# Kernel optimization log

Hardware: AMD Instinct MI355X
Metric: run time of the kernel (lower is better)

Reference implementation:

```python
import jax, jax.numpy as jnp
import numpy as np

H, DM, N, K, R = 768, 1536, 16, 4, 48  # hidden, intermediate, state, conv kernel, dt rank
B, L = 2, 1024


def _silu(x):
    return x * jax.nn.sigmoid(x)


def _causal_conv(x, w, b):
    # x: [B, D, L]; w: [D, K] depthwise; causal left-pad K-1 (matches causal_conv1d_fn)
    out = jax.lax.conv_general_dilated(
        x, w[:, None, :], window_strides=(1,), padding=[(K - 1, 0)],
        feature_group_count=w.shape[0], dimension_numbers=('NCH', 'OIH', 'NCH'))
    return out + b[None, :, None]


def _selective_scan(u, delta, A, Bm, Cm, Dp, gate):
    # u/delta/gate: [B, D, L]; A: [D, N]; Bm/Cm: [B, L, N]; Dp: [D]
    dA = jnp.exp(delta[:, :, :, None] * A[None, :, None, :])              # [B,D,L,N]
    dBu = delta[:, :, :, None] * Bm[:, None, :, :] * u[:, :, :, None]      # [B,D,L,N]
    dA_t = jnp.moveaxis(dA, 2, 0)    # [L,B,D,N]
    dBu_t = jnp.moveaxis(dBu, 2, 0)  # [L,B,D,N]
    C_t = jnp.moveaxis(Cm, 1, 0)     # [L,B,N]

    def step(x, inp):
        a, bu, c = inp
        x = a * x + bu                               # [B,D,N]
        y = jnp.einsum('bdn,bn->bd', x, c)
        return x, y

    x0 = jnp.zeros(dA_t.shape[1:], dA_t.dtype)
    _, ys = jax.lax.scan(step, x0, (dA_t, dBu_t, C_t))
    y = jnp.moveaxis(ys, 0, 2) + u * Dp[None, :, None]   # [B,D,L]
    return y * _silu(gate)


def _branch(conv_out, gate, xw, dtw, dtb, Alog, Dp):
    # conv_out/gate: [B, D, L]
    ssm = jnp.einsum('bdl,pd->blp', conv_out, xw)        # [B,L,R+2N]
    ts, Bm, Cm = ssm[..., :R], ssm[..., R:R + N], ssm[..., R + N:]
    delta = jax.nn.softplus(jnp.einsum('dr,blr->bdl', dtw, ts) + dtb[None, :, None])
    A = -jnp.exp(Alog)
    return _selective_scan(conv_out, delta, A, Bm, Cm, Dp, gate)


def setup_inputs() -> dict:
    key = jax.random.key(0)
    ks = jax.random.split(key, 12)
    s = 0.02
    hidden_states = jax.random.normal(ks[0], (B, L, H), jnp.float32)
    in_proj_w = jax.random.normal(ks[1], (2 * DM, H), jnp.float32) * s
    conv_w = jax.random.normal(ks[2], (DM, K), jnp.float32) * 0.3
    conv_b = jax.random.normal(ks[3], (DM,), jnp.float32) * s
    x_proj_w = jax.random.normal(ks[4], (R + 2 * N, DM), jnp.float32) * s
    dt_proj_w = jax.random.normal(ks[5], (DM, R), jnp.float32) * s
    dt_proj_b = -4.0 + 0.1 * jax.random.normal(ks[6], (DM,), jnp.float32)
    x_proj_back_w = jax.random.normal(ks[7], (R + 2 * N, DM), jnp.float32) * s
    dt_proj_back_w = jax.random.normal(ks[8], (DM, R), jnp.float32) * s
    dt_proj_back_b = -4.0 + 0.1 * jax.random.normal(ks[9], (DM,), jnp.float32)
    A_log = jnp.log(jnp.broadcast_to(jnp.arange(1, N + 1, dtype=jnp.float32)[None, :], (DM, N)))
    A_log_back = A_log
    D = jnp.ones((DM,), jnp.float32)
    D_back = jnp.ones((DM,), jnp.float32)
    out_proj_w = jax.random.normal(ks[10], (H, DM), jnp.float32) * s
    return {
        'hidden_states': hidden_states, 'in_proj_w': in_proj_w,
        'conv_w': conv_w, 'conv_b': conv_b,
        'x_proj_w': x_proj_w, 'dt_proj_w': dt_proj_w, 'dt_proj_b': dt_proj_b,
        'x_proj_back_w': x_proj_back_w, 'dt_proj_back_w': dt_proj_back_w,
        'dt_proj_back_b': dt_proj_back_b, 'A_log': A_log, 'A_log_back': A_log_back,
        'D': D, 'D_back': D_back, 'out_proj_w': out_proj_w,
    }


def reference(hidden_states, in_proj_w, conv_w, conv_b, x_proj_w, dt_proj_w,
              dt_proj_b, x_proj_back_w, dt_proj_back_w, dt_proj_back_b,
              A_log, A_log_back, D, D_back, out_proj_w):
    proj = jnp.einsum('blh,ph->bpl', hidden_states, in_proj_w)  # [B,2D,L]
    x, gate = proj[:, :DM], proj[:, DM:]
    conv_out = _silu(_causal_conv(x, conv_w, conv_b))           # [B,D,L]
    # forward-direction scan
    y_f = _branch(conv_out, gate, x_proj_w, dt_proj_w, dt_proj_b, A_log, D)
    # backward-direction scan on time-flipped conv output and gate
    y_b = _branch(conv_out[:, :, ::-1], gate[:, :, ::-1], x_proj_back_w,
                  dt_proj_back_w, dt_proj_back_b, A_log_back, D_back)
    y = y_f + y_b[:, :, ::-1]
    return jnp.einsum('bdl,hd->blh', y, out_proj_w)
```

## Files before the change

### kernel.cpp

```cpp
#include <hip/hip_runtime.h>
#include <math.h>

constexpr int cH  = 768;
constexpr int cDM = 1536;
constexpr int cN  = 16;
constexpr int cR  = 48;
constexpr int cB  = 2;
constexpr int cL  = 1024;
constexpr int cPS = 160;
constexpr int cCK = 8;

typedef unsigned short u16;
typedef __attribute__((ext_vector_type(8))) short bf16x8;
typedef __attribute__((ext_vector_type(4))) float f32x4;

__device__ __forceinline__ u16 f2bf(float f) {
    unsigned u = __float_as_uint(f);
    u += 0x7FFF + ((u >> 16) & 1);
    return (u16)(u >> 16);
}
__device__ __forceinline__ float bf2f(u16 h) {
    return __uint_as_float((unsigned)h << 16);
}

__device__ __forceinline__ float row16_sum(float y) {
    int v;
    v = __builtin_amdgcn_update_dpp(0, __float_as_int(y), 0xB1, 0xF, 0xF, true);
    y += __int_as_float(v);
    v = __builtin_amdgcn_update_dpp(0, __float_as_int(y), 0x4E, 0xF, 0xF, true);
    y += __int_as_float(v);
    v = __builtin_amdgcn_update_dpp(0, __float_as_int(y), 0x141, 0xF, 0xF, true);
    y += __int_as_float(v);
    v = __builtin_amdgcn_update_dpp(0, __float_as_int(y), 0x140, 0xF, 0xF, true);
    y += __int_as_float(v);
    return y;
}

__global__ __launch_bounds__(256)
void prep_kernel(const float* __restrict__ hid, const float* __restrict__ inw,
                 const float* __restrict__ xpw, const float* __restrict__ xpbw,
                 const float* __restrict__ outw, const float* __restrict__ dtw,
                 const float* __restrict__ dtbw,
                 u16* __restrict__ hid_b, u16* __restrict__ inw_b,
                 u16* __restrict__ xpw2_b, u16* __restrict__ outw_b,
                 u16* __restrict__ dtw2_b)
{
    const long i8 = ((long)blockIdx.x * 256 + threadIdx.x) * 8;
    const long e0 = 1572864;
    const long e1 = e0 + 2359296;
    const long e2 = e1 + 122880;
    const long e3 = e2 + 122880;
    const long e4 = e3 + 1179648;
    const long e5 = e4 + 98304;
    const long e6 = e5 + 98304;
    const float* in; u16* out; long off; int pad = 0;
    if      (i8 < e0) { in = hid;  out = hid_b;           off = i8; }
    else if (i8 < e1) { in = inw;  out = inw_b;           off = i8 - e0; }
    else if (i8 < e2) { in = xpw;  out = xpw2_b;          off = i8 - e1; }
    else if (i8 < e3) { in = xpbw; out = xpw2_b + 122880; off = i8 - e2; }
    else if (i8 < e4) { in = outw; out = outw_b;          off = i8 - e3; }
    else if (i8 < e5) { in = dtw;  out = dtw2_b;          off = i8 - e4; pad = 1; }
    else if (i8 < e6) { in = dtbw; out = dtw2_b + 98304;  off = i8 - e5; pad = 1; }
    else return;
    u16 o[8];
    if (!pad) {
        const float4 a = *(const float4*)&in[off];
        const float4 b = *(const float4*)&in[off + 4];
        o[0]=f2bf(a.x); o[1]=f2bf(a.y); o[2]=f2bf(a.z); o[3]=f2bf(a.w);
        o[4]=f2bf(b.x); o[5]=f2bf(b.y); o[6]=f2bf(b.z); o[7]=f2bf(b.w);
    } else {
        const long r = off >> 6; const int k0 = (int)(off & 63);
        #pragma unroll
        for (int k = 0; k < 8; ++k)
            o[k] = (k0 + k < cR) ? f2bf(in[r * cR + k0 + k]) : (u16)0;
    }
    *(uint4*)&out[off] = *(uint4*)o;
}

__global__ __launch_bounds__(256)
void tspad_kernel(const float* __restrict__ ssms, u16* __restrict__ out) {
    int i = blockIdx.x * 256 + threadIdx.x;
    int dirsel = i >> 17;
    int rem = i & 131071;
    int bl = rem >> 6, k = rem & 63;
    out[i] = (k < cR) ? f2bf(ssms[(long)bl * cPS + dirsel * 80 + k]) : (u16)0;
}

__global__ __launch_bounds__(256)
void comb_kernel(u16* __restrict__ yf, const u16* __restrict__ yb, long n8) {
    long i = (long)blockIdx.x * 256 + threadIdx.x;
    if (i >= n8) return;
    uint4 av = ((uint4*)yf)[i];
    uint4 bv = ((const uint4*)yb)[i];
    unsigned* ap = (unsigned*)&av;
    unsigned* bp = (unsigned*)&bv;
    #pragma unroll
    for (int j = 0; j < 4; ++j) {
        const float lo = bf2f((u16)(ap[j] & 0xffff)) + bf2f((u16)(bp[j] & 0xffff));
        const float hi = bf2f((u16)(ap[j] >> 16))    + bf2f((u16)(bp[j] >> 16));
        ap[j] = (unsigned)f2bf(lo) | ((unsigned)f2bf(hi) << 16);
    }
    ((uint4*)yf)[i] = av;
}

__device__ __forceinline__ void gld_lds16(const u16* g, u16* l) {
    __builtin_amdgcn_global_load_lds(
        (const __attribute__((address_space(1))) unsigned int*)g,
        (__attribute__((address_space(3))) unsigned int*)l, 16, 0, 0);
}

#define GST(SA, SB, k0) do {                                                   \
    _Pragma("unroll")                                                          \
    for (int h = 0; h < 3; ++h) {                                              \
        const int q  = wid * 3 + h;                                            \
        const int rw = lane >> 2;                                              \
        if (q < 4) {                                                           \
            const int r  = q * 16 + rw;                                        \
            const int sw = (r & 3) ^ ((r >> 2) & 3);                           \
            const int kg = (k0) + (((lane & 3) ^ sw) << 3);                    \
            gld_lds16(Ab + (long)(m0 + r) * lda + kg, &SA[q * 512]);           \
        } else {                                                               \
            const int r  = (q - 4) * 16 + rw;                                  \
            const int sw = (r & 3) ^ ((r >> 2) & 3);                           \
            const int kg = (k0) + (((lane & 3) ^ sw) << 3);                    \
            int nr = n0 + r; if (nr > N2 - 1) nr = N2 - 1;                     \
            gld_lds16(Bb + (long)nr * ldb + kg, &SB[(q - 4) * 512]);           \
        }                                                                      \
    }                                                                          \
} while (0)

#define CMP(SA, SB) do {                                                       \
    bf16x8 af[4], bfr[2];                                                      \
    _Pragma("unroll")                                                          \
    for (int i = 0; i < 4; ++i) {                                              \
        const int ra  = i * 16 + lr;                                           \
        const int swa = (ra & 3) ^ ((ra >> 2) & 3);                            \
        af[i] = *(const bf16x8*)&SA[ra * 32 + ((lc ^ swa) << 3)];              \
    }                                                                          \
    _Pragma("unroll")                                                          \
    for (int j = 0; j < 2; ++j) {                                              \
        const int rb  = wn + j * 16 + lr;                                      \
        const int swb = (rb & 3) ^ ((rb >> 2) & 3);                            \
        bfr[j] = *(const bf16x8*)&SB[rb * 32 + ((lc ^ swb) << 3)];             \
    }                                                                          \
    _Pragma("unroll")                                                          \
    for (int i = 0; i < 4; ++i)                                                \
        _Pragma("unroll")                                                      \
        for (int j = 0; j < 2; ++j)                                            \
            acc[i][j] = __builtin_amdgcn_mfma_f32_16x16x32_bf16(af[i], bfr[j], acc[i][j], 0, 0, 0); \
} while (0)

template<int EPI>
__global__ __launch_bounds__(256, 4)
void gemm_mfma(const u16* __restrict__ A, const u16* __restrict__ B,
               const u16* __restrict__ B_hi,
               float* __restrict__ C0, float* __restrict__ C1,
               const float* __restrict__ bias, const float* __restrict__ bias_hi,
               int N2, int Kd, int lda, int ldb, int ldc,
               long sA, long sB, long sC, int splitRow, int kspl)
{
    __shared__ __align__(16) u16 shA0[2048];
    __shared__ __align__(16) u16 shA1[2048];
    __shared__ __align__(16) u16 shB0[4096];
    __shared__ __align__(16) u16 shB1[4096];
    const int tid  = threadIdx.x;
    const int wid  = tid >> 6, lane = tid & 63;
    const int lr   = lane & 15, lc = lane >> 4;
    const int z    = blockIdx.z;
    const int bz   = z / kspl, ks = z % kspl;
    const int kpc  = Kd / kspl;
    const int kbeg = ks * kpc;
    const int nt   = kpc / 32;
    const int n0 = blockIdx.x * 128, m0 = blockIdx.y * 64;
    const int wn = wid * 32;

    const u16* Bsel = (B_hi != nullptr && m0 >= splitRow) ? B_hi : B;
    const float* biasp = (bias_hi != nullptr && m0 >= splitRow) ? bias_hi : bias;
    const int mro = (bias_hi != nullptr && m0 >= splitRow) ? splitRow : 0;

    const u16* Ab = A + (long)bz * sA;
    const u16* Bb = Bsel + (long)bz * sB;

    f32x4 acc[4][2] = {};

    GST(shA0, shB0, kbeg);
    __syncthreads();
    int t = 0;
    for (;;) {
        if (t + 1 < nt) GST(shA1, shB1, kbeg + (t + 1) * 32);
        CMP(shA0, shB0);
        __syncthreads();
        if (++t >= nt) break;
        if (t + 1 < nt) GST(shA0, shB0, kbeg + (t + 1) * 32);
        CMP(shA1, shB1);
        __syncthreads();
        if (++t >= nt) break;
    }

    #pragma unroll
    for (int i = 0; i < 4; ++i) {
        #pragma unroll
        for (int e = 0; e < 4; ++e) {
            const int m = m0 + i * 16 + lc * 4 + e;
            float* crow;
            if (C1 != nullptr && m >= splitRow)
                crow = C1 + (long)bz * sC + (long)(m - splitRow) * ldc;
            else
                crow = C0 + (long)bz * sC + (long)m * ldc;
            const float bi = (EPI == 1) ? biasp[m - mro] : 0.f;
            #pragma unroll
            for (int j = 0; j < 2; ++j) {
                const int n = n0 + wn + j * 16 + lr;
                if (n < N2) {
                    float v = acc[i][j][e];
                    if (EPI == 1) {
                        const float t2 = v + bi;
                        v = fmaxf(t2, 0.f) + __logf(1.f + __expf(-fabsf(t2)));
                    }
                    if (EPI == 2) atomicAdd(crow + n, v);
                    else          crow[n] = v;
                }
            }
        }
    }
}

__global__ __launch_bounds__(256)
void conv_silu_t(const float* __restrict__ x, const float* __restrict__ cw,
                 const float* __restrict__ cb,
                 float* __restrict__ conv, u16* __restrict__ convT)
{
    __shared__ float xs_[32][36];
    __shared__ float cs[32][33];
    const int l0 = blockIdx.x * 32, d0 = blockIdx.y * 32, b = blockIdx.z;
    const int lx = threadIdx.x & 31, dy = threadIdx.x >> 5;

    #pragma unroll
    for (int r = 0; r < 4; ++r) {
        const int dd = dy + r * 8;
        const float* xr = x + ((long)b * cDM + d0 + dd) * cL;
        const int li = l0 - 3 + lx;
        xs_[dd][lx] = (li >= 0) ? xr[li] : 0.f;
        if (lx < 3) xs_[dd][32 + lx] = xr[l0 + 29 + lx];
    }
    __syncthreads();
    #pragma unroll
    for (int r = 0; r < 4; ++r) {
        const int dd = dy + r * 8;
        const int d = d0 + dd;
        const float w0 = cw[d*4], w1 = cw[d*4+1], w2 = cw[d*4+2], w3 = cw[d*4+3];
        float v = cb[d];
        v = fmaf(w0, xs_[dd][lx],     v);
        v = fmaf(w1, xs_[dd][lx + 1], v);
        v = fmaf(w2, xs_[dd][lx + 2], v);
        v = fmaf(w3, xs_[dd][lx + 3], v);
        const float s = v / (1.f + __expf(-v));
        conv[((long)b * cDM + d) * cL + l0 + lx] = s;
        cs[lx][dd] = s;
    }
    __syncthreads();
    #pragma unroll
    for (int r = 0; r < 4; ++r) {
        const int ll = dy + r * 8;
        convT[((long)b * cL + l0 + ll) * cDM + d0 + lx] = f2bf(cs[ll][lx]);
    }
}

#define SC_LOAD(w) do {                                                       \
    const int ta_ = tb0 + (w) * 32;                                           \
    const int lb_ = dir ? (cL - 1 - (ta_ + t_bc)) : (ta_ + t_bc);             \
    rbc = *(const float4*)&sp[(long)lb_ * cPS + sofs + cc0];                  \
    const int tu_ = ta_ + 2 * n;                                              \
    if (!dir) {                                                               \
        ru2 = *(const float2*)&up[tu_];                                       \
        rd2 = *(const float2*)&dp[tu_];                                       \
    } else {                                                                  \
        const float2 a_ = *(const float2*)&up[cL - 2 - tu_];                  \
        const float2 b_ = *(const float2*)&dp[cL - 2 - tu_];                  \
        ru2 = make_float2(a_.y, a_.x);                                        \
        rd2 = make_float2(b_.y, b_.x);                                        \
    }                                                                         \
} while (0)

#define SC_WRITE(bufi) do {                                                   \
    bcS[bufi][cc0 + 0][t_bc] = rbc.x;                                         \
    bcS[bufi][cc0 + 1][t_bc] = rbc.y;                                         \
    bcS[bufi][cc0 + 2][t_bc] = rbc.z;                                         \
    bcS[bufi][cc0 + 3][t_bc] = rbc.w;                                         \
    *(float2*)&dS[bufi][g][2 * n]   = rd2;                                    \
    *(float2*)&duuS[bufi][g][2 * n] = make_float2(rd2.x * ru2.x, rd2.y * ru2.y); \
} while (0)

__global__ __launch_bounds__(256)
void scanA_kernel(const float* __restrict__ conv,
                  const float* __restrict__ delta_f,
                  const float* __restrict__ delta_b,
                  const float* __restrict__ ssms,
                  const float* __restrict__ Alog_f,
                  const float* __restrict__ Alog_b,
                  float* __restrict__ Ap_out, float* __restrict__ Xf_out)
{
    __shared__ float bcS[2][32][36];
    __shared__ float dS[2][16][36];
    __shared__ float duuS[2][16][36];

    const int tid = threadIdx.x;
    const int g = tid >> 4, n = tid & 15;
    const int d = blockIdx.x * 16 + g;
    const int b = blockIdx.y;
    const int z = blockIdx.z;
    const int dir = z >> 3, ck = z & 7;

    const float* delta = dir ? delta_b : delta_f;
    const float* Alog  = dir ? Alog_b  : Alog_f;
    const float a = -__expf(Alog[d * cN + n]);
    const int sofs = dir ? 128 : 48;

    const int t_bc = tid >> 3;
    const int cc0  = (tid & 7) << 2;
    const int tb0  = ck * (cL / cCK);

    const float* up = conv  + ((long)b * cDM + d) * cL;
    const float* dp = delta + ((long)b * cDM + d) * cL;
    const float* sp = ssms + (long)b * cL * cPS;

    float4 rbc; float2 ru2, rd2;
    SC_LOAD(0);
    SC_WRITE(0);
    __syncthreads();

    float xs = 0.f, Ap = 1.f;
    for (int w = 0; w < (cL / cCK) / 32; ++w) {
        const int cur = w & 1;
        if (w < (cL / cCK) / 32 - 1) SC_LOAD(w + 1);

        #pragma unroll
        for (int s = 0; s < 4; ++s) {
            const int t0 = s * 8;
            const float4 b0  = *(const float4*)&bcS[cur][n][t0];
            const float4 b1  = *(const float4*)&bcS[cur][n][t0 + 4];
            const float4 dd0 = *(const float4*)&dS[cur][g][t0];
            const float4 dd1 = *(const float4*)&dS[cur][g][t0 + 4];
            const float4 uu0 = *(const float4*)&duuS[cur][g][t0];
            const float4 uu1 = *(const float4*)&duuS[cur][g][t0 + 4];
            float dA[8], dBu[8];
            dA[0]=__expf(dd0.x*a); dA[1]=__expf(dd0.y*a); dA[2]=__expf(dd0.z*a); dA[3]=__expf(dd0.w*a);
            dA[4]=__expf(dd1.x*a); dA[5]=__expf(dd1.y*a); dA[6]=__expf(dd1.z*a); dA[7]=__expf(dd1.w*a);
            dBu[0]=uu0.x*b0.x; dBu[1]=uu0.y*b0.y; dBu[2]=uu0.z*b0.z; dBu[3]=uu0.w*b0.w;
            dBu[4]=uu1.x*b1.x; dBu[5]=uu1.y*b1.y; dBu[6]=uu1.z*b1.z; dBu[7]=uu1.w*b1.w;
            #pragma unroll
            for (int k = 0; k < 8; ++k) {
                xs = fmaf(dA[k], xs, dBu[k]);
                Ap *= dA[k];
            }
        }
        if (w < (cL / cCK) / 32 - 1) SC_WRITE(cur ^ 1);
        __syncthreads();
    }
    const long idx = (((long)(b * 2 + dir) * cDM + d) * cCK + ck) * 16 + n;
    Ap_out[idx] = Ap;
    Xf_out[idx] = xs;
}

__global__ __launch_bounds__(256)
void scanB_kernel(const float* __restrict__ Ap, const float* __restrict__ Xf,
                  float* __restrict__ X0)
{
    const int gid = blockIdx.x * 256 + threadIdx.x;
    const int n = gid & 15;
    const long s = gid >> 4;
    float x0 = 0.f;
    #pragma unroll
    for (int c = 0; c < cCK; ++c) {
        const long idx = (s * cCK + c) * 16 + n;
        X0[idx] = x0;
        x0 = fmaf(Ap[idx], x0, Xf[idx]);
    }
}

__global__ __launch_bounds__(256)
void scanC_kernel(const float* __restrict__ conv,
                  const float* __restrict__ gate,
                  const float* __restrict__ delta_f,
                  const float* __restrict__ delta_b,
                  const float* __restrict__ ssms,
                  const float* __restrict__ Alog_f,
                  const float* __restrict__ Alog_b,
                  const float* __restrict__ D_f, const float* __restrict__ D_b,
                  const float* __restrict__ X0,
                  u16* __restrict__ yf, u16* __restrict__ yb)
{
    __shared__ float bcS[2][32][36];
    __shared__ float dS[2][16][36];
    __shared__ float duuS[2][16][36];

    const int tid = threadIdx.x;
    const int g = tid >> 4, n = tid & 15;
    const int d = blockIdx.x * 16 + g;
    const int b = blockIdx.y;
    const int z = blockIdx.z;
    const int dir = z >> 3, ck = z & 7;

    const float* delta = dir ? delta_b : delta_f;
    const float* Alog  = dir ? Alog_b  : Alog_f;
    const float  Dd    = dir ? D_b[d]  : D_f[d];
    u16*         yout  = dir ? yb      : yf;
    const float  a     = -__expf(Alog[d * cN + n]);
    const int    sofs  = dir ? 128 : 48;

    const int t_bc = tid >> 3;
    const int cc0  = (tid & 7) << 2;
    const int tb0  = ck * (cL / cCK);

    const float* up = conv  + ((long)b * cDM + d) * cL;
    const float* gp = gate  + ((long)b * cDM + d) * cL;
    const float* dp = delta + ((long)b * cDM + d) * cL;
    const float* sp = ssms + (long)b * cL * cPS;

    float xs = X0[(((long)(b * 2 + dir) * cDM + d) * cCK + ck) * 16 + n];

    float4 rbc; float2 ru2, rd2;
    SC_LOAD(0);
    SC_WRITE(0);
    __syncthreads();

    for (int w = 0; w < (cL / cCK) / 32; ++w) {
        const int cur = w & 1;
        if (w < (cL / cCK) / 32 - 1) SC_LOAD(w + 1);

        #pragma unroll
        for (int s = 0; s < 4; ++s) {
            const int t0 = s * 8;
            const float4 b0  = *(const float4*)&bcS[cur][n][t0];
            const float4 b1  = *(const float4*)&bcS[cur][n][t0 + 4];
            const float4 c0  = *(const float4*)&bcS[cur][16 + n][t0];
            const float4 c1  = *(const float4*)&bcS[cur][16 + n][t0 + 4];
            const float4 dd0 = *(const float4*)&dS[cur][g][t0];
            const float4 dd1 = *(const float4*)&dS[cur][g][t0 + 4];
            const float4 uu0 = *(const float4*)&duuS[cur][g][t0];
            const float4 uu1 = *(const float4*)&duuS[cur][g][t0 + 4];
            float dA[8], dBu[8], C8[8];
            dA[0]=__expf(dd0.x*a); dA[1]=__expf(dd0.y*a); dA[2]=__expf(dd0.z*a); dA[3]=__expf(dd0.w*a);
            dA[4]=__expf(dd1.x*a); dA[5]=__expf(dd1.y*a); dA[6]=__expf(dd1.z*a); dA[7]=__expf(dd1.w*a);
            dBu[0]=uu0.x*b0.x; dBu[1]=uu0.y*b0.y; dBu[2]=uu0.z*b0.z; dBu[3]=uu0.w*b0.w;
            dBu[4]=uu1.x*b1.x; dBu[5]=uu1.y*b1.y; dBu[6]=uu1.z*b1.z; dBu[7]=uu1.w*b1.w;
            C8[0]=c0.x; C8[1]=c0.y; C8[2]=c0.z; C8[3]=c0.w;
            C8[4]=c1.x; C8[5]=c1.y; C8[6]=c1.z; C8[7]=c1.w;

            float yo = 0.f;
            #pragma unroll
            for (int k = 0; k < 8; ++k) {
                xs = fmaf(dA[k], xs, dBu[k]);
                const float y = row16_sum(xs * C8[k]);
                if (n == k) yo = y;
            }
            if (n < 8) {
                const int wt = tb0 + w * 32 + t0 + n;
                const int l  = dir ? (cL - 1 - wt) : wt;
                const float uu = up[l];
                const float gv = gp[l];
                const float val = (yo + uu * Dd) * (gv / (1.f + __expf(-gv)));
                yout[((long)b * cL + l) * cDM + d] = f2bf(val);
            }
        }
        if (w < (cL / cCK) / 32 - 1) SC_WRITE(cur ^ 1);
        __syncthreads();
    }
}

extern "C" void kernel_launch(void* const* d_in, const int* in_sizes, int n_in,
                              void* d_out, int out_size, void* d_ws, size_t ws_size,
                              hipStream_t stream)
{
    const float* hid   = (const float*)d_in[0];
    const float* inw   = (const float*)d_in[1];
    const float* convw = (const float*)d_in[2];
    const float* convb = (const float*)d_in[3];
    const float* xpw   = (const float*)d_in[4];
    const float* dtw   = (const float*)d_in[5];
    const float* dtb   = (const float*)d_in[6];
    const float* xpbw  = (const float*)d_in[7];
    const float* dtbw  = (const float*)d_in[8];
    const float* dtbb  = (const float*)d_in[9];
    const float* Alog  = (const float*)d_in[10];
    const float* Alogb = (const float*)d_in[11];
    const float* Dv    = (const float*)d_in[12];
    const float* Dbv   = (const float*)d_in[13];
    const float* outw  = (const float*)d_in[14];
    float* out = (float*)d_out;

    float* ws = (float*)d_ws;
    const long S = (long)cB * cDM * cL;
    float* xbuf   = ws;
    float* gate   = ws + S;
    float* conv   = ws + 2 * S;
    float* deltab = ws + 3 * S;
    float* ssms   = ws + 4 * S;
    u16* up0      = (u16*)(ssms + (long)cB * cL * cPS);
    u16* convT_b  = up0;
    u16* ts2_b    = up0 + S;
    u16* xpw2_b   = ts2_b + (long)2 * cB * cL * 64;
    u16* dtw2_b   = xpw2_b + (long)cPS * cDM;
    u16* outw_b   = dtw2_b + (long)2 * cDM * 64;
    u16* pool2    = outw_b + (long)cH * cDM;
    u16* inw_b    = pool2;
    u16* hid_b    = pool2 + (long)2 * cDM * cH;
    u16* yf_b     = convT_b;
    u16* yb_b     = pool2;
    const long nSum = (long)2 * cB * cDM * cCK * 16;
    float* sumAp  = (float*)(pool2 + 3932160);
    float* sumXf  = sumAp + nSum;
    float* sumX0  = sumXf + nSum;

    const dim3 blk(256);

    prep_kernel<<<dim3(2713), blk, 0, stream>>>(
        hid, inw, xpw, xpbw, outw, dtw, dtbw,
        hid_b, inw_b, xpw2_b, outw_b, dtw2_b);

    hipMemsetAsync(ssms, 0, (long)cB * cL * cPS * sizeof(float), stream);
    hipMemsetAsync(out, 0, (long)out_size * sizeof(float), stream);

    gemm_mfma<0><<<dim3(cL / 128, (2 * cDM) / 64, cB), blk, 0, stream>>>(
        inw_b, hid_b, nullptr, xbuf, gate, nullptr, nullptr,
        cL, cH, cH, cH, cL, 0L, (long)cL * cH, (long)cDM * cL, cDM, 1);

    conv_silu_t<<<dim3(cL / 32, cDM / 32, cB), blk, 0, stream>>>(
        xbuf, convw, convb, conv, convT_b);

    gemm_mfma<2><<<dim3(2, cL / 64, cB * 8), blk, 0, stream>>>(
        convT_b, xpw2_b, nullptr, ssms, nullptr, nullptr, nullptr,
        cPS, cDM, cDM, cDM, cPS, (long)cL * cDM, 0L, (long)cL * cPS, 1 << 30, 8);

    tspad_kernel<<<1024, blk, 0, stream>>>(ssms, ts2_b);

    gemm_mfma<1><<<dim3(cL / 128, (2 * cDM) / 64, cB), blk, 0, stream>>>(
        dtw2_b, ts2_b, ts2_b + (long)cB * cL * 64,
        xbuf , deltab, dtb, dtbb,
        cL, 64, 64, 64, cL, 0L, (long)cL * 64, (long)cDM * cL, cDM, 1);

    scanA_kernel<<<dim3(cDM / 16, cB, 2 * cCK), blk, 0, stream>>>(
        conv, xbuf , deltab, ssms, Alog, Alogb, sumAp, sumXf);
    scanB_kernel<<<dim3(384), blk, 0, stream>>>(sumAp, sumXf, sumX0);
    scanC_kernel<<<dim3(cDM / 16, cB, 2 * cCK), blk, 0, stream>>>(
        conv, gate, xbuf , deltab, ssms,
        Alog, Alogb, Dv, Dbv, sumX0, yf_b, yb_b);

    comb_kernel<<<(int)(S / 8 / 256), blk, 0, stream>>>(yf_b, yb_b, S / 8);

    gemm_mfma<2><<<dim3(cH / 128, cL / 64, cB * 2), blk, 0, stream>>>(
        yf_b, outw_b, nullptr, out, nullptr, nullptr, nullptr,
        cH, cDM, cDM, cDM, cH, (long)cL * cDM, 0L, (long)cL * cH, 1 << 30, 2);
}
```

Before: 187.6 us.

## Switch to time-major layout and thread-per-channel chunked scan with more chunks

Activations are now stored time-major ([B,L,D]) by swapping the GEMM operand roles, so conv, delta, gate and u are contiguous across channels. The scan kernels map one thread to one channel holding all 16 states in registers, which removes the DPP row reductions and shared-memory staging. The chunk count rises from 8 to 32 for more parallelism. The per-thread register load goes up and the scanB pass over the chunk carries gets longer.

```diff
diff --git a/kernel.cpp b/kernel.cpp
--- a/kernel.cpp
+++ b/kernel.cpp
@@ -8,7 +8,7 @@
 constexpr int cB  = 2;
 constexpr int cL  = 1024;
 constexpr int cPS = 160;
-constexpr int cCK = 8;
+constexpr int cCK = 32;
 
 typedef unsigned short u16;
 typedef __attribute__((ext_vector_type(8))) short bf16x8;
@@ -21,19 +21,6 @@
 }
 __device__ __forceinline__ float bf2f(u16 h) {
     return __uint_as_float((unsigned)h << 16);
-}
-
-__device__ __forceinline__ float row16_sum(float y) {
-    int v;
-    v = __builtin_amdgcn_update_dpp(0, __float_as_int(y), 0xB1, 0xF, 0xF, true);
-    y += __int_as_float(v);
-    v = __builtin_amdgcn_update_dpp(0, __float_as_int(y), 0x4E, 0xF, 0xF, true);
-    y += __int_as_float(v);
-    v = __builtin_amdgcn_update_dpp(0, __float_as_int(y), 0x141, 0xF, 0xF, true);
-    y += __int_as_float(v);
-    v = __builtin_amdgcn_update_dpp(0, __float_as_int(y), 0x140, 0xF, 0xF, true);
-    y += __int_as_float(v);
-    return y;
 }
 
 __global__ __launch_bounds__(256)
@@ -153,11 +140,10 @@
 template<int EPI>
 __global__ __launch_bounds__(256, 4)
 void gemm_mfma(const u16* __restrict__ A, const u16* __restrict__ B,
-               const u16* __restrict__ B_hi,
                float* __restrict__ C0, float* __restrict__ C1,
-               const float* __restrict__ bias, const float* __restrict__ bias_hi,
+               const float* __restrict__ bias,
                int N2, int Kd, int lda, int ldb, int ldc,
-               long sA, long sB, long sC, int splitRow, int kspl)
+               long sA, long sC, int splitCol, int kspl)
 {
     __shared__ __align__(16) u16 shA0[2048];
     __shared__ __align__(16) u16 shA1[2048];
@@ -174,12 +160,8 @@
     const int n0 = blockIdx.x * 128, m0 = blockIdx.y * 64;
     const int wn = wid * 32;
 
-    const u16* Bsel = (B_hi != nullptr && m0 >= splitRow) ? B_hi : B;
-    const float* biasp = (bias_hi != nullptr && m0 >= splitRow) ? bias_hi : bias;
-    const int mro = (bias_hi != nullptr && m0 >= splitRow) ? splitRow : 0;
-
     const u16* Ab = A + (long)bz * sA;
-    const u16* Bb = Bsel + (long)bz * sB;
+    const u16* Bb = B;
 
     f32x4 acc[4][2] = {};
 
@@ -202,23 +184,21 @@
         #pragma unroll
         for (int e = 0; e < 4; ++e) {
             const int m = m0 + i * 16 + lc * 4 + e;
-            float* crow;
-            if (C1 != nullptr && m >= splitRow)
-                crow = C1 + (long)bz * sC + (long)(m - splitRow) * ldc;
-            else
-                crow = C0 + (long)bz * sC + (long)m * ldc;
-            const float bi = (EPI == 1) ? biasp[m - mro] : 0.f;
+            float* base0 = C0 + (long)bz * sC + (long)m * ldc;
+            float* base1 = (C1 != nullptr) ? C1 + (long)bz * sC + (long)m * ldc : nullptr;
             #pragma unroll
             for (int j = 0; j < 2; ++j) {
                 const int n = n0 + wn + j * 16 + lr;
                 if (n < N2) {
                     float v = acc[i][j][e];
                     if (EPI == 1) {
-                        const float t2 = v + bi;
+                        const float t2 = v + bias[n];
                         v = fmaxf(t2, 0.f) + __logf(1.f + __expf(-fabsf(t2)));
                     }
-                    if (EPI == 2) atomicAdd(crow + n, v);
-                    else          crow[n] = v;
+                    float* cp = (base1 && n >= splitCol) ? base1 + (n - splitCol)
+                                                         : base0 + n;
+                    if (EPI == 2) atomicAdd(cp, v);
+                    else          *cp = v;
                 }
             }
         }
@@ -226,145 +206,124 @@
 }
 
 __global__ __launch_bounds__(256)
-void conv_silu_t(const float* __restrict__ x, const float* __restrict__ cw,
-                 const float* __restrict__ cb,
-                 float* __restrict__ conv, u16* __restrict__ convT)
-{
-    __shared__ float xs_[32][36];
-    __shared__ float cs[32][33];
-    const int l0 = blockIdx.x * 32, d0 = blockIdx.y * 32, b = blockIdx.z;
-    const int lx = threadIdx.x & 31, dy = threadIdx.x >> 5;
-
-    #pragma unroll
-    for (int r = 0; r < 4; ++r) {
-        const int dd = dy + r * 8;
-        const float* xr = x + ((long)b * cDM + d0 + dd) * cL;
-        const int li = l0 - 3 + lx;
-        xs_[dd][lx] = (li >= 0) ? xr[li] : 0.f;
-        if (lx < 3) xs_[dd][32 + lx] = xr[l0 + 29 + lx];
+void conv_silu2(const float* __restrict__ x, const float* __restrict__ cw,
+                const float* __restrict__ cb,
+                float* __restrict__ convTf, u16* __restrict__ convT_b)
+{
+    __shared__ float xt[35][64];
+    const int l0 = blockIdx.x * 32, d0 = blockIdx.y * 64, b = blockIdx.z;
+    const int tid = threadIdx.x;
+    for (int i = tid; i < 35 * 64; i += 256) {
+        const int r = i >> 6, c = i & 63;
+        const int l = l0 - 3 + r;
+        xt[r][c] = (l >= 0) ? x[((long)b * cL + l) * cDM + d0 + c] : 0.f;
     }
     __syncthreads();
-    #pragma unroll
-    for (int r = 0; r < 4; ++r) {
-        const int dd = dy + r * 8;
-        const int d = d0 + dd;
-        const float w0 = cw[d*4], w1 = cw[d*4+1], w2 = cw[d*4+2], w3 = cw[d*4+3];
-        float v = cb[d];
-        v = fmaf(w0, xs_[dd][lx],     v);
-        v = fmaf(w1, xs_[dd][lx + 1], v);
-        v = fmaf(w2, xs_[dd][lx + 2], v);
-        v = fmaf(w3, xs_[dd][lx + 3], v);
+    const int dc = tid & 63, lsub = tid >> 6;
+    const int d = d0 + dc;
+    const float w0 = cw[d*4], w1 = cw[d*4+1], w2 = cw[d*4+2], w3 = cw[d*4+3];
+    const float bi = cb[d];
+    #pragma unroll
+    for (int k = 0; k < 8; ++k) {
+        const int row = lsub * 8 + k;
+        float v = bi;
+        v = fmaf(w0, xt[row][dc],     v);
+        v = fmaf(w1, xt[row + 1][dc], v);
+        v = fmaf(w2, xt[row + 2][dc], v);
+        v = fmaf(w3, xt[row + 3][dc], v);
         const float s = v / (1.f + __expf(-v));
-        conv[((long)b * cDM + d) * cL + l0 + lx] = s;
-        cs[lx][dd] = s;
-    }
-    __syncthreads();
-    #pragma unroll
-    for (int r = 0; r < 4; ++r) {
-        const int ll = dy + r * 8;
-        convT[((long)b * cL + l0 + ll) * cDM + d0 + lx] = f2bf(cs[ll][lx]);
-    }
-}
-
-#define SC_LOAD(w) do {                                                       \
-    const int ta_ = tb0 + (w) * 32;                                           \
-    const int lb_ = dir ? (cL - 1 - (ta_ + t_bc)) : (ta_ + t_bc);             \
-    rbc = *(const float4*)&sp[(long)lb_ * cPS + sofs + cc0];                  \
-    const int tu_ = ta_ + 2 * n;                                              \
-    if (!dir) {                                                               \
-        ru2 = *(const float2*)&up[tu_];                                       \
-        rd2 = *(const float2*)&dp[tu_];                                       \
-    } else {                                                                  \
-        const float2 a_ = *(const float2*)&up[cL - 2 - tu_];                  \
-        const float2 b_ = *(const float2*)&dp[cL - 2 - tu_];                  \
-        ru2 = make_float2(a_.y, a_.x);                                        \
-        rd2 = make_float2(b_.y, b_.x);                                        \
-    }                                                                         \
-} while (0)
-
-#define SC_WRITE(bufi) do {                                                   \
-    bcS[bufi][cc0 + 0][t_bc] = rbc.x;                                         \
-    bcS[bufi][cc0 + 1][t_bc] = rbc.y;                                         \
-    bcS[bufi][cc0 + 2][t_bc] = rbc.z;                                         \
-    bcS[bufi][cc0 + 3][t_bc] = rbc.w;                                         \
-    *(float2*)&dS[bufi][g][2 * n]   = rd2;                                    \
-    *(float2*)&duuS[bufi][g][2 * n] = make_float2(rd2.x * ru2.x, rd2.y * ru2.y); \
-} while (0)
-
-__global__ __launch_bounds__(256)
-void scanA_kernel(const float* __restrict__ conv,
-                  const float* __restrict__ delta_f,
-                  const float* __restrict__ delta_b,
-                  const float* __restrict__ ssms,
-                  const float* __restrict__ Alog_f,
-                  const float* __restrict__ Alog_b,
+        const long o = ((long)b * cL + l0 + row) * cDM + d;
+        convTf[o] = s;
+        convT_b[o] = f2bf(s);
+    }
+}
+
+#define SA_LOADG(g, DU, UU) _Pragma("unroll")                                  \
+    for (int k = 0; k < 8; ++k) {                                              \
+        const int t_ = (g) * 8 + k;                                            \
+        const int l_ = dir ? (base - t_) : (base + t_);                        \
+        const long off_ = (long)l_ * cDM + d;                                  \
+        DU[k] = dT[off_]; UU[k] = uT[off_];                                    \
+    }
+
+#define SA_COMP(g, DU, UU) _Pragma("unroll")                                   \
+    for (int k = 0; k < 8; ++k) {                                              \
+        const int t_ = (g) * 8 + k;                                            \
+        const float du_ = DU[k]; const float duu_ = du_ * UU[k];               \
+        const float4 b0_ = *(const float4*)&bcA[t_][0];                        \
+        const float4 b1_ = *(const float4*)&bcA[t_][4];                        \
+        const float4 b2_ = *(const float4*)&bcA[t_][8];                        \
+        const float4 b3_ = *(const float4*)&bcA[t_][12];                       \
+        const float bb_[16] = {b0_.x,b0_.y,b0_.z,b0_.w, b1_.x,b1_.y,b1_.z,b1_.w, \
+                               b2_.x,b2_.y,b2_.z,b2_.w, b3_.x,b3_.y,b3_.z,b3_.w}; \
+        _Pragma("unroll")                                                      \
+        for (int n = 0; n < 16; ++n) {                                         \
+            const float dA_ = __expf(du_ * a[n]);                              \
+            xs[n] = fmaf(dA_, xs[n], duu_ * bb_[n]);                           \
+            Ap[n] *= dA_;                                                      \
+        }                                                                      \
+    }
+
+__global__ __launch_bounds__(64, 4)
+void scanA_kernel(const float* __restrict__ dT0, const float* __restrict__ dT1,
+                  const float* __restrict__ uF, const float* __restrict__ ssms,
+                  const float* __restrict__ AlogF, const float* __restrict__ AlogB,
                   float* __restrict__ Ap_out, float* __restrict__ Xf_out)
 {
-    __shared__ float bcS[2][32][36];
-    __shared__ float dS[2][16][36];
-    __shared__ float duuS[2][16][36];
-
-    const int tid = threadIdx.x;
-    const int g = tid >> 4, n = tid & 15;
-    const int d = blockIdx.x * 16 + g;
+    __shared__ float bcA[32][16];
+    const int lane = threadIdx.x;
+    const int d = blockIdx.x * 64 + lane;
     const int b = blockIdx.y;
     const int z = blockIdx.z;
-    const int dir = z >> 3, ck = z & 7;
-
-    const float* delta = dir ? delta_b : delta_f;
-    const float* Alog  = dir ? Alog_b  : Alog_f;
-    const float a = -__expf(Alog[d * cN + n]);
+    const int dir = z >> 5, ck = z & 31;
+    const float* Alog = dir ? AlogB : AlogF;
+    const float* dT = (dir ? dT1 : dT0) + (long)b * cL * cDM;
+    const float* uT = uF + (long)b * cL * cDM;
+    const float* sp = ssms + (long)b * cL * cPS;
     const int sofs = dir ? 128 : 48;
-
-    const int t_bc = tid >> 3;
-    const int cc0  = (tid & 7) << 2;
-    const int tb0  = ck * (cL / cCK);
-
-    const float* up = conv  + ((long)b * cDM + d) * cL;
-    const float* dp = delta + ((long)b * cDM + d) * cL;
-    const float* sp = ssms + (long)b * cL * cPS;
-
-    float4 rbc; float2 ru2, rd2;
-    SC_LOAD(0);
-    SC_WRITE(0);
+    const int base = dir ? (cL - 1 - ck * 32) : (ck * 32);
+
+    #pragma unroll
+    for (int h = 0; h < 2; ++h) {
+        const int idx = h * 64 + lane;
+        const int r = idx >> 2, q = idx & 3;
+        const int lr_ = dir ? (base - r) : (base + r);
+        *(float4*)&bcA[r][q * 4] = *(const float4*)&sp[(long)lr_ * cPS + sofs + q * 4];
+    }
+    float a[16];
+    #pragma unroll
+    for (int h = 0; h < 4; ++h) {
+        const float4 av = *(const float4*)&Alog[d * 16 + h * 4];
+        a[h*4+0] = -__expf(av.x); a[h*4+1] = -__expf(av.y);
+        a[h*4+2] = -__expf(av.z); a[h*4+3] = -__expf(av.w);
+    }
     __syncthreads();
 
-    float xs = 0.f, Ap = 1.f;
-    for (int w = 0; w < (cL / cCK) / 32; ++w) {
-        const int cur = w & 1;
-        if (w < (cL / cCK) / 32 - 1) SC_LOAD(w + 1);
-
-        #pragma unroll
-        for (int s = 0; s < 4; ++s) {
-            const int t0 = s * 8;
-            const float4 b0  = *(const float4*)&bcS[cur][n][t0];
-            const float4 b1  = *(const float4*)&bcS[cur][n][t0 + 4];
-            const float4 dd0 = *(const float4*)&dS[cur][g][t0];
-            const float4 dd1 = *(const float4*)&dS[cur][g][t0 + 4];
-            const float4 uu0 = *(const float4*)&duuS[cur][g][t0];
-            const float4 uu1 = *(const float4*)&duuS[cur][g][t0 + 4];
-            float dA[8], dBu[8];
-            dA[0]=__expf(dd0.x*a); dA[1]=__expf(dd0.y*a); dA[2]=__expf(dd0.z*a); dA[3]=__expf(dd0.w*a);
-            dA[4]=__expf(dd1.x*a); dA[5]=__expf(dd1.y*a); dA[6]=__expf(dd1.z*a); dA[7]=__expf(dd1.w*a);
-            dBu[0]=uu0.x*b0.x; dBu[1]=uu0.y*b0.y; dBu[2]=uu0.z*b0.z; dBu[3]=uu0.w*b0.w;
-            dBu[4]=uu1.x*b1.x; dBu[5]=uu1.y*b1.y; dBu[6]=uu1.z*b1.z; dBu[7]=uu1.w*b1.w;
-            #pragma unroll
-            for (int k = 0; k < 8; ++k) {
-                xs = fmaf(dA[k], xs, dBu[k]);
-                Ap *= dA[k];
-            }
-        }
-        if (w < (cL / cCK) / 32 - 1) SC_WRITE(cur ^ 1);
-        __syncthreads();
-    }
-    const long idx = (((long)(b * 2 + dir) * cDM + d) * cCK + ck) * 16 + n;
-    Ap_out[idx] = Ap;
-    Xf_out[idx] = xs;
+    float xs[16] = {};
+    float Ap[16];
+    #pragma unroll
+    for (int n = 0; n < 16; ++n) Ap[n] = 1.f;
+
+    float duA[8], uuA[8], duB[8], uuB[8];
+    SA_LOADG(0, duA, uuA);
+    SA_LOADG(1, duB, uuB);
+    SA_COMP(0, duA, uuA);
+    SA_LOADG(2, duA, uuA);
+    SA_COMP(1, duB, uuB);
+    SA_LOADG(3, duB, uuB);
+    SA_COMP(2, duA, uuA);
+    SA_COMP(3, duB, uuB);
+
+    const long ob = (((long)(b * 2 + dir) * cDM + d) * cCK + ck) * 16;
+    #pragma unroll
+    for (int h = 0; h < 4; ++h) {
+        *(float4*)&Ap_out[ob + h * 4] = make_float4(Ap[h*4], Ap[h*4+1], Ap[h*4+2], Ap[h*4+3]);
+        *(float4*)&Xf_out[ob + h * 4] = make_float4(xs[h*4], xs[h*4+1], xs[h*4+2], xs[h*4+3]);
+    }
 }
 
 __global__ __launch_bounds__(256)
-void scanB_kernel(const float* __restrict__ Ap, const float* __restrict__ Xf,
-                  float* __restrict__ X0)
+void scanB_kernel(float* __restrict__ Ap, const float* __restrict__ Xf)
 {
     const int gid = blockIdx.x * 256 + threadIdx.x;
     const int n = gid & 15;
@@ -373,99 +332,107 @@
     #pragma unroll
     for (int c = 0; c < cCK; ++c) {
         const long idx = (s * cCK + c) * 16 + n;
-        X0[idx] = x0;
-        x0 = fmaf(Ap[idx], x0, Xf[idx]);
-    }
-}
-
-__global__ __launch_bounds__(256)
-void scanC_kernel(const float* __restrict__ conv,
-                  const float* __restrict__ gate,
-                  const float* __restrict__ delta_f,
-                  const float* __restrict__ delta_b,
+        const float ap = Ap[idx], xf = Xf[idx];
+        Ap[idx] = x0;
+        x0 = fmaf(ap, x0, xf);
+    }
+}
+
+#define SC_LOADG(g, DU, UU, GV) _Pragma("unroll")                              \
+    for (int k = 0; k < 8; ++k) {                                              \
+        const int t_ = (g) * 8 + k;                                            \
+        const int l_ = dir ? (base - t_) : (base + t_);                        \
+        const long off_ = (long)l_ * cDM + d;                                  \
+        DU[k] = dT[off_]; UU[k] = uT[off_]; GV[k] = gT[off_];                  \
+    }
+
+#define SC_COMP(g, DU, UU, GV) _Pragma("unroll")                               \
+    for (int k = 0; k < 8; ++k) {                                              \
+        const int t_ = (g) * 8 + k;                                            \
+        const float du_ = DU[k]; const float uu_ = UU[k];                      \
+        const float duu_ = du_ * uu_;                                          \
+        const float4 b0_ = *(const float4*)&bc[t_][0];                         \
+        const float4 b1_ = *(const float4*)&bc[t_][4];                         \
+        const float4 b2_ = *(const float4*)&bc[t_][8];                         \
+        const float4 b3_ = *(const float4*)&bc[t_][12];                        \
+        const float4 c0_ = *(const float4*)&bc[t_][16];                        \
+        const float4 c1_ = *(const float4*)&bc[t_][20];                        \
+        const float4 c2_ = *(const float4*)&bc[t_][24];                        \
+        const float4 c3_ = *(const float4*)&bc[t_][28];                        \
+        const float bb_[16] = {b0_.x,b0_.y,b0_.z,b0_.w, b1_.x,b1_.y,b1_.z,b1_.w, \
+                               b2_.x,b2_.y,b2_.z,b2_.w, b3_.x,b3_.y,b3_.z,b3_.w}; \
+        const float cc_[16] = {c0_.x,c0_.y,c0_.z,c0_.w, c1_.x,c1_.y,c1_.z,c1_.w, \
+                               c2_.x,c2_.y,c2_.z,c2_.w, c3_.x,c3_.y,c3_.z,c3_.w}; \
+        float y_ = 0.f;                                                        \
+        _Pragma("unroll")                                                      \
+        for (int n = 0; n < 16; ++n) {                                         \
+            const float dA_ = __expf(du_ * a[n]);                              \
+            xs[n] = fmaf(dA_, xs[n], duu_ * bb_[n]);                           \
+            y_ = fmaf(xs[n], cc_[n], y_);                                      \
+        }                                                                      \
+        const int l2_ = dir ? (base - t_) : (base + t_);                       \
+        const float gv_ = GV[k];                                               \
+        const float val_ = (y_ + uu_ * Dd) * (gv_ / (1.f + __expf(-gv_)));     \
+        yout[((long)b * cL + l2_) * cDM + d] = f2bf(val_);                     \
+    }
+
+__global__ __launch_bounds__(64, 4)
+void scanC_kernel(const float* __restrict__ dT0, const float* __restrict__ dT1,
+                  const float* __restrict__ uF, const float* __restrict__ gF,
                   const float* __restrict__ ssms,
-                  const float* __restrict__ Alog_f,
-                  const float* __restrict__ Alog_b,
-                  const float* __restrict__ D_f, const float* __restrict__ D_b,
+                  const float* __restrict__ AlogF, const float* __restrict__ AlogB,
+                  const float* __restrict__ Df, const float* __restrict__ Db,
                   const float* __restrict__ X0,
                   u16* __restrict__ yf, u16* __restrict__ yb)
 {
-    __shared__ float bcS[2][32][36];
-    __shared__ float dS[2][16][36];
-    __shared__ float duuS[2][16][36];
-
-    const int tid = threadIdx.x;
-    const int g = tid >> 4, n = tid & 15;
-    const int d = blockIdx.x * 16 + g;
+    __shared__ float bc[32][32];
+    const int lane = threadIdx.x;
+    const int d = blockIdx.x * 64 + lane;
     const int b = blockIdx.y;
     const int z = blockIdx.z;
-    const int dir = z >> 3, ck = z & 7;
-
-    const float* delta = dir ? delta_b : delta_f;
-    const float* Alog  = dir ? Alog_b  : Alog_f;
-    const float  Dd    = dir ? D_b[d]  : D_f[d];
-    u16*         yout  = dir ? yb      : yf;
-    const float  a     = -__expf(Alog[d * cN + n]);
-    const int    sofs  = dir ? 128 : 48;
-
-    const int t_bc = tid >> 3;
-    const int cc0  = (tid & 7) << 2;
-    const int tb0  = ck * (cL / cCK);
-
-    const float* up = conv  + ((long)b * cDM + d) * cL;
-    const float* gp = gate  + ((long)b * cDM + d) * cL;
-    const float* dp = delta + ((long)b * cDM + d) * cL;
+    const int dir = z >> 5, ck = z & 31;
+    const float* Alog = dir ? AlogB : AlogF;
+    const float* dT = (dir ? dT1 : dT0) + (long)b * cL * cDM;
+    const float* uT = uF + (long)b * cL * cDM;
+    const float* gT = gF + (long)b * cL * cDM;
     const float* sp = ssms + (long)b * cL * cPS;
-
-    float xs = X0[(((long)(b * 2 + dir) * cDM + d) * cCK + ck) * 16 + n];
-
-    float4 rbc; float2 ru2, rd2;
-    SC_LOAD(0);
-    SC_WRITE(0);
+    const float Dd = dir ? Db[d] : Df[d];
+    u16* yout = dir ? yb : yf;
+    const int sofs = dir ? 128 : 48;
+    const int base = dir ? (cL - 1 - ck * 32) : (ck * 32);
+
+    #pragma unroll
+    for (int h = 0; h < 4; ++h) {
+        const int idx = h * 64 + lane;
+        const int r = idx >> 3, q = idx & 7;
+        const int lr_ = dir ? (base - r) : (base + r);
+        *(float4*)&bc[r][q * 4] = *(const float4*)&sp[(long)lr_ * cPS + sofs + q * 4];
+    }
+    float a[16];
+    #pragma unroll
+    for (int h = 0; h < 4; ++h) {
+        const float4 av = *(const float4*)&Alog[d * 16 + h * 4];
+        a[h*4+0] = -__expf(av.x); a[h*4+1] = -__expf(av.y);
+        a[h*4+2] = -__expf(av.z); a[h*4+3] = -__expf(av.w);
+    }
+    float xs[16];
+    const long ob = (((long)(b * 2 + dir) * cDM + d) * cCK + ck) * 16;
+    #pragma unroll
+    for (int h = 0; h < 4; ++h) {
+        const float4 xv = *(const float4*)&X0[ob + h * 4];
+        xs[h*4+0] = xv.x; xs[h*4+1] = xv.y; xs[h*4+2] = xv.z; xs[h*4+3] = xv.w;
+    }
     __syncthreads();
 
-    for (int w = 0; w < (cL / cCK) / 32; ++w) {
-        const int cur = w & 1;
-        if (w < (cL / cCK) / 32 - 1) SC_LOAD(w + 1);
-
-        #pragma unroll
-        for (int s = 0; s < 4; ++s) {
-            const int t0 = s * 8;
-            const float4 b0  = *(const float4*)&bcS[cur][n][t0];
-            const float4 b1  = *(const float4*)&bcS[cur][n][t0 + 4];
-            const float4 c0  = *(const float4*)&bcS[cur][16 + n][t0];
-            const float4 c1  = *(const float4*)&bcS[cur][16 + n][t0 + 4];
-            const float4 dd0 = *(const float4*)&dS[cur][g][t0];
-            const float4 dd1 = *(const float4*)&dS[cur][g][t0 + 4];
-            const float4 uu0 = *(const float4*)&duuS[cur][g][t0];
-            const float4 uu1 = *(const float4*)&duuS[cur][g][t0 + 4];
-            float dA[8], dBu[8], C8[8];
-            dA[0]=__expf(dd0.x*a); dA[1]=__expf(dd0.y*a); dA[2]=__expf(dd0.z*a); dA[3]=__expf(dd0.w*a);
-            dA[4]=__expf(dd1.x*a); dA[5]=__expf(dd1.y*a); dA[6]=__expf(dd1.z*a); dA[7]=__expf(dd1.w*a);
-            dBu[0]=uu0.x*b0.x; dBu[1]=uu0.y*b0.y; dBu[2]=uu0.z*b0.z; dBu[3]=uu0.w*b0.w;
-            dBu[4]=uu1.x*b1.x; dBu[5]=uu1.y*b1.y; dBu[6]=uu1.z*b1.z; dBu[7]=uu1.w*b1.w;
-            C8[0]=c0.x; C8[1]=c0.y; C8[2]=c0.z; C8[3]=c0.w;
-            C8[4]=c1.x; C8[5]=c1.y; C8[6]=c1.z; C8[7]=c1.w;
-
-            float yo = 0.f;
-            #pragma unroll
-            for (int k = 0; k < 8; ++k) {
-                xs = fmaf(dA[k], xs, dBu[k]);
-                const float y = row16_sum(xs * C8[k]);
-                if (n == k) yo = y;
-            }
-            if (n < 8) {
-                const int wt = tb0 + w * 32 + t0 + n;
-                const int l  = dir ? (cL - 1 - wt) : wt;
-                const float uu = up[l];
-                const float gv = gp[l];
-                const float val = (yo + uu * Dd) * (gv / (1.f + __expf(-gv)));
-                yout[((long)b * cL + l) * cDM + d] = f2bf(val);
-            }
-        }
-        if (w < (cL / cCK) / 32 - 1) SC_WRITE(cur ^ 1);
-        __syncthreads();
-    }
+    float duA[8], uuA[8], gvA[8], duB[8], uuB[8], gvB[8];
+    SC_LOADG(0, duA, uuA, gvA);
+    SC_LOADG(1, duB, uuB, gvB);
+    SC_COMP(0, duA, uuA, gvA);
+    SC_LOADG(2, duA, uuA, gvA);
+    SC_COMP(1, duB, uuB, gvB);
+    SC_LOADG(3, duB, uuB, gvB);
+    SC_COMP(2, duA, uuA, gvA);
+    SC_COMP(3, duB, uuB, gvB);
 }
 
 extern "C" void kernel_launch(void* const* d_in, const int* in_sizes, int n_in,
@@ -493,8 +460,8 @@
     const long S = (long)cB * cDM * cL;
     float* xbuf   = ws;
     float* gate   = ws + S;
-    float* conv   = ws + 2 * S;
-    float* deltab = ws + 3 * S;
+    float* convTf = ws + 2 * S;
+    float* deltaT1= ws + 3 * S;
     float* ssms   = ws + 4 * S;
     u16* up0      = (u16*)(ssms + (long)cB * cL * cPS);
     u16* convT_b  = up0;
@@ -510,7 +477,6 @@
     const long nSum = (long)2 * cB * cDM * cCK * 16;
     float* sumAp  = (float*)(pool2 + 3932160);
     float* sumXf  = sumAp + nSum;
-    float* sumX0  = sumXf + nSum;
 
     const dim3 blk(256);
 
@@ -521,34 +487,36 @@
     hipMemsetAsync(ssms, 0, (long)cB * cL * cPS * sizeof(float), stream);
     hipMemsetAsync(out, 0, (long)out_size * sizeof(float), stream);
 
-    gemm_mfma<0><<<dim3(cL / 128, (2 * cDM) / 64, cB), blk, 0, stream>>>(
-        inw_b, hid_b, nullptr, xbuf, gate, nullptr, nullptr,
-        cL, cH, cH, cH, cL, 0L, (long)cL * cH, (long)cDM * cL, cDM, 1);
-
-    conv_silu_t<<<dim3(cL / 32, cDM / 32, cB), blk, 0, stream>>>(
-        xbuf, convw, convb, conv, convT_b);
-
-    gemm_mfma<2><<<dim3(2, cL / 64, cB * 8), blk, 0, stream>>>(
-        convT_b, xpw2_b, nullptr, ssms, nullptr, nullptr, nullptr,
-        cPS, cDM, cDM, cDM, cPS, (long)cL * cDM, 0L, (long)cL * cPS, 1 << 30, 8);
+    gemm_mfma<0><<<dim3(24, 16, cB), blk, 0, stream>>>(
+        hid_b, inw_b, xbuf, gate, nullptr,
+        2 * cDM, cH, cH, cH, cDM, (long)cL * cH, (long)cL * cDM, cDM, 1);
+
+    conv_silu2<<<dim3(32, 24, cB), blk, 0, stream>>>(
+        xbuf, convw, convb, convTf, convT_b);
+
+    gemm_mfma<2><<<dim3(2, 16, cB * 8), blk, 0, stream>>>(
+        convT_b, xpw2_b, ssms, nullptr, nullptr,
+        cPS, cDM, cDM, cDM, cPS, (long)cL * cDM, (long)cL * cPS, 1 << 30, 8);
 
     tspad_kernel<<<1024, blk, 0, stream>>>(ssms, ts2_b);
 
-    gemm_mfma<1><<<dim3(cL / 128, (2 * cDM) / 64, cB), blk, 0, stream>>>(
-        dtw2_b, ts2_b, ts2_b + (long)cB * cL * 64,
-        xbuf , deltab, dtb, dtbb,
-        cL, 64, 64, 64, cL, 0L, (long)cL * 64, (long)cDM * cL, cDM, 1);
-
-    scanA_kernel<<<dim3(cDM / 16, cB, 2 * cCK), blk, 0, stream>>>(
-        conv, xbuf , deltab, ssms, Alog, Alogb, sumAp, sumXf);
-    scanB_kernel<<<dim3(384), blk, 0, stream>>>(sumAp, sumXf, sumX0);
-    scanC_kernel<<<dim3(cDM / 16, cB, 2 * cCK), blk, 0, stream>>>(
-        conv, gate, xbuf , deltab, ssms,
-        Alog, Alogb, Dv, Dbv, sumX0, yf_b, yb_b);
+    gemm_mfma<1><<<dim3(12, 16, cB), blk, 0, stream>>>(
+        ts2_b, dtw2_b, xbuf, nullptr, dtb,
+        cDM, 64, 64, 64, cDM, (long)cL * 64, (long)cL * cDM, 1 << 30, 1);
+    gemm_mfma<1><<<dim3(12, 16, cB), blk, 0, stream>>>(
+        ts2_b + (long)2 * cL * 64, dtw2_b + (long)cDM * 64, deltaT1, nullptr, dtbb,
+        cDM, 64, 64, 64, cDM, (long)cL * 64, (long)cL * cDM, 1 << 30, 1);
+
+    scanA_kernel<<<dim3(24, cB, 2 * cCK), dim3(64), 0, stream>>>(
+        xbuf, deltaT1, convTf, ssms, Alog, Alogb, sumAp, sumXf);
+    scanB_kernel<<<dim3(384), blk, 0, stream>>>(sumAp, sumXf);
+    scanC_kernel<<<dim3(24, cB, 2 * cCK), dim3(64), 0, stream>>>(
+        xbuf, deltaT1, convTf, gate, ssms, Alog, Alogb, Dv, Dbv,
+        sumAp , yf_b, yb_b);
 
     comb_kernel<<<(int)(S / 8 / 256), blk, 0, stream>>>(yf_b, yb_b, S / 8);
 
-    gemm_mfma<2><<<dim3(cH / 128, cL / 64, cB * 2), blk, 0, stream>>>(
-        yf_b, outw_b, nullptr, out, nullptr, nullptr, nullptr,
-        cH, cDM, cDM, cDM, cH, (long)cL * cDM, 0L, (long)cL * cH, 1 << 30, 2);
-}
+    gemm_mfma<2><<<dim3(6, 16, cB * 2), blk, 0, stream>>>(
+        yf_b, outw_b, out, nullptr, nullptr,
+        cH, cDM, cDM, cDM, cH, (long)cL * cDM, (long)cL * cH, 1 << 30, 2);
+}
```

After: 363.7 us. 93.9% more time.
